# Kernel optimization log

Measured on AMD Instinct MI355X. Metric: run time of the kernel, lower is better.

The kernel has to match this reference:

```python
import jax, jax.numpy as jnp
import numpy as np

D = 256
H = 8
DH = D // H
TANH_CLIP = 10.0
NEG_INF = -1e9


def setup_inputs() -> dict:
    key = jax.random.key(0)
    ks = jax.random.split(key, 7)
    B, T, N = 32, 512, 512
    s = 1.0 / np.sqrt(D)
    return {
        "embeddings": jax.random.normal(ks[0], (B, N, D), dtype=jnp.float32),
        "current_nodes": jax.random.randint(ks[1], (B, T), 0, N, dtype=jnp.int64),
        "action_mask": jax.random.randint(ks[2], (B, T, N), 0, 2) > 0,
        "W_node": jax.random.normal(ks[3], (D, 3 * D), dtype=jnp.float32) * s,
        "W_fixed": jax.random.normal(ks[4], (D, D), dtype=jnp.float32) * s,
        "W_step": jax.random.normal(ks[5], (D, D), dtype=jnp.float32) * s,
        "W_out": jax.random.normal(ks[6], (D, D), dtype=jnp.float32) * s,
    }


def reference(embeddings, current_nodes, action_mask, W_node, W_fixed, W_step, W_out):
    """Batched equivalent of the autoregressive pointer-attention decode loop.

    embeddings: [B, N, D]; current_nodes: [B, T]; action_mask: [B, T, N] (True = feasible).
    Returns log_p: [B, T, N].
    """
    B, N, _ = embeddings.shape
    # ---- _precompute_cache ----
    proj = embeddings @ W_node                      # [B, N, 3D]
    glimpse_k, glimpse_v, logit_k = jnp.split(proj, 3, axis=-1)
    graph_context = jnp.mean(embeddings, axis=1) @ W_fixed   # [B, D]

    # ---- step context (gather current node embedding, project) ----
    step_emb = jnp.take_along_axis(embeddings, current_nodes[..., None], axis=1)  # [B, T, D]
    glimpse_q = step_emb @ W_step + graph_context[:, None, :]                      # [B, T, D]

    # ---- multi-head glimpse attention (one query per decode step) ----
    q = glimpse_q.reshape(B, -1, H, DH)
    k = glimpse_k.reshape(B, N, H, DH)
    v = glimpse_v.reshape(B, N, H, DH)
    scores = jnp.einsum("bthd,bnhd->bhtn", q, k) / np.sqrt(DH)
    scores = jnp.where(action_mask[:, None, :, :], scores, NEG_INF)
    attn = jax.nn.softmax(scores, axis=-1)
    heads = jnp.einsum("bhtn,bnhd->bthd", attn, v).reshape(B, -1, D)
    glimpse = heads @ W_out                                                        # [B, T, D]

    # ---- pointer logits: tanh clipping, mask, log-softmax ----
    logits = jnp.einsum("btd,bnd->btn", glimpse, logit_k) / np.sqrt(D)
    logits = TANH_CLIP * jnp.tanh(logits)
    logits = jnp.where(action_mask, logits, NEG_INF)
    return jax.nn.log_softmax(logits, axis=-1)
```

## Files before the change

### kernel.cpp

```cpp
#include <hip/hip_runtime.h>
#include <hip/hip_bf16.h>

constexpr int BB = 32;
constexpr int TT = 512;
constexpr int NN = 512;
constexpr int DD = 256;
constexpr int HH = 8;
constexpr int DH = 32;
#define NEG_INF (-1e9f)

typedef __attribute__((ext_vector_type(8))) short bf16x8;
typedef __attribute__((ext_vector_type(4))) float f32x4;

__device__ inline ushort f2bf(float x) {
    union { float f; unsigned u; } c; c.f = x;
    unsigned u = c.u + 0x7fffu + ((c.u >> 16) & 1u);
    return (ushort)(u >> 16);
}
__device__ inline uint pk2t(float a, float b) {
    return __builtin_amdgcn_perm(__float_as_uint(b), __float_as_uint(a),
                                 0x07060302u);
}
__device__ inline ushort tr16(float x) { return (ushort)(__float_as_uint(x) >> 16); }
__device__ inline float bf2f(ushort u) {
    union { uint u; float f; } c; c.u = (uint)u << 16; return c.f;
}
__device__ inline float fast_tanh10(float x) {
    x = fminf(fmaxf(x, -20.f), 20.f);
    float e2 = __expf(2.f * x);
    return 10.f * (1.f - 2.f / (e2 + 1.f));
}

__global__ __launch_bounds__(256) void prep_all_k(
    const float* __restrict__ emb, ushort* __restrict__ embB,
    float* __restrict__ partial, const float* __restrict__ Wn,
    const float* __restrict__ Ws, const float* __restrict__ Wo,
    ushort* __restrict__ WnT, ushort* __restrict__ WsT,
    ushort* __restrict__ WoT, const int* __restrict__ mask,
    uint* __restrict__ mbt) {
    int j = blockIdx.x;
    int tid = threadIdx.x;
    if (j < 256) {
        int b = j >> 3, part = j & 7, d = tid;
        const float* eb = emb + ((size_t)b * NN + part * 64) * DD + d;
        ushort* ob = embB + ((size_t)b * NN + part * 64) * DD + d;
        float s = 0.f;
        #pragma unroll 4
        for (int i = 0; i < 64; i++) {
            float v = eb[(size_t)i * DD];
            s += v;
            ob[(size_t)i * DD] = f2bf(v);
        }
        partial[((size_t)b * 8 + part) * DD + d] = s;
    } else if (j < 576) {
        __shared__ float t[32][33];
        int g = j - 256;
        int gx = g % 40, gy = g / 40;
        const float* W;
        ushort* WT;
        int NC, xb;
        if (gx < 24)      { W = Wn; WT = WnT; NC = 768; xb = gx; }
        else if (gx < 32) { W = Ws; WT = WsT; NC = 256; xb = gx - 24; }
        else              { W = Wo; WT = WoT; NC = 256; xb = gx - 32; }
        int tx = tid & 31, ty = tid >> 5;
        int x = xb * 32 + tx;
        int y0 = gy * 32;
        #pragma unroll
        for (int i = 0; i < 4; i++)
            t[ty + i * 8][tx] = W[(size_t)(y0 + ty + i * 8) * NC + x];
        __syncthreads();
        #pragma unroll
        for (int i = 0; i < 4; i++)
            WT[(size_t)(xb * 32 + ty + i * 8) * 256 + y0 + tx] =
                f2bf(t[tx][ty + i * 8]);
    } else {
        int idx = (j - 576) * 256 + tid;
        int row = idx >> 4, w = idx & 15;
        const int* mr = mask + (size_t)row * NN + w;
        uint u = 0;
        #pragma unroll
        for (int c = 0; c < 32; c++) u |= (uint)(mr[c * 16] != 0) << c;
        mbt[idx] = u;
    }
}

template <int TASK>
__global__ __launch_bounds__(256) void gemm3_k(
    const ushort* __restrict__ A0, const ushort* __restrict__ WT0,
    const ushort* __restrict__ WT1, ushort* __restrict__ O0,
    ushort* __restrict__ O1, ushort* __restrict__ O2,
    ushort* __restrict__ O3, const float* __restrict__ partial,
    const float* __restrict__ Wf, const int* __restrict__ cur) {
    int j = blockIdx.x;
    bool k2 = (TASK == 0) && (j >= 1536);
    int bx, by;
    if (TASK == 0 && !k2) {
        int x = j & 7, t = j >> 3;
        bx = x * 16 + t / 12; by = t % 12;
    } else {
        int jj = k2 ? j - 1536 : j;
        int x = jj & 7, t = jj >> 3;
        bx = x * 16 + (t >> 2); by = t & 3;
    }
    int row0 = bx * 128, col0 = by * 64;
    int tid = threadIdx.x;
    int w = tid >> 6, l = tid & 63;
    int lo = l & 15, hi = l >> 4;

    __shared__ ushort As[128 * 64];
    __shared__ ushort Bs[64 * 64];
    __shared__ float ctxs[64];

    const ushort* WT = k2 ? WT1 : WT0;
    const f32x4 zero = {0.f, 0.f, 0.f, 0.f};
    f32x4 acc[2][4] = {{zero, zero, zero, zero}, {zero, zero, zero, zero}};

    for (int kk = 0; kk < 4; kk++) {
        if (kk) __syncthreads();
        #pragma unroll
        for (int i = 0; i < 4; i++) {
            int u = i * 256 + tid;
            int row = u >> 3, slot = u & 7;
            int arow = row0 + row;
            const ushort* ap;
            if (k2) {
                int b = arow >> 9;
                ap = A0 + ((size_t)(b * NN + cur[arow])) * DD;
            } else {
                ap = A0 + (size_t)arow * DD;
            }
            uint4 v = *(const uint4*)(ap + kk * 64 + slot * 8);
            *(uint4*)((char*)As + row * 128 + ((slot ^ (row & 7)) << 4)) = v;
        }
        #pragma unroll
        for (int i = 0; i < 2; i++) {
            int u = i * 256 + tid;
            int row = u >> 3, slot = u & 7;
            uint4 v = *(const uint4*)(WT + (size_t)(col0 + row) * 256 + kk * 64 + slot * 8);
            *(uint4*)((char*)Bs + row * 128 + ((slot ^ (row & 7)) << 4)) = v;
        }
        __syncthreads();
        #pragma unroll
        for (int ks = 0; ks < 2; ks++) {
            int sx = ((ks * 4 + hi) ^ (lo & 7)) << 4;
            bf16x8 af0 = *(const bf16x8*)((char*)As + (w * 32 + lo) * 128 + sx);
            bf16x8 af1 = *(const bf16x8*)((char*)As + (w * 32 + 16 + lo) * 128 + sx);
            #pragma unroll
            for (int c = 0; c < 4; c++) {
                bf16x8 bf = *(const bf16x8*)((char*)Bs + (c * 16 + lo) * 128 + sx);
                acc[0][c] = __builtin_amdgcn_mfma_f32_16x16x32_bf16(af0, bf, acc[0][c], 0, 0, 0);
                acc[1][c] = __builtin_amdgcn_mfma_f32_16x16x32_bf16(af1, bf, acc[1][c], 0, 0, 0);
            }
        }
    }

    int bbq = row0 >> 9;
    if (k2) {
        __syncthreads();
        float* fs = (float*)As;
        float mk = 0.f;
        #pragma unroll
        for (int p = 0; p < 8; p++)
            mk += partial[(size_t)bbq * 2048 + p * 256 + tid];
        fs[tid] = mk * (1.0f / 512.0f);
        __syncthreads();
        int cc = tid & 63, part = tid >> 6;
        float cs = 0.f;
        #pragma unroll 16
        for (int k = part * 64; k < part * 64 + 64; k++)
            cs += fs[k] * Wf[(size_t)k * 256 + col0 + cc];
        float* fs2 = fs + 256;
        fs2[part * 64 + cc] = cs;
        __syncthreads();
        if (tid < 64)
            ctxs[tid] = fs2[tid] + fs2[64 + tid] + fs2[128 + tid] + fs2[192 + tid];
        __syncthreads();
    }

    #pragma unroll
    for (int rg = 0; rg < 2; rg++) {
        int rw0 = row0 + w * 32 + rg * 16;
        int bb = rw0 >> 9;
        #pragma unroll
        for (int c = 0; c < 4; c++) {
            int col = col0 + c * 16 + lo;
            float v[4];
            #pragma unroll
            for (int r = 0; r < 4; r++) v[r] = acc[rg][c][r];
            if constexpr (TASK == 0) {
                if (k2) {
                    float bv = ctxs[col - col0];
                    #pragma unroll
                    for (int r = 0; r < 4; r++)
                        O3[(size_t)(rw0 + 4 * hi + r) * DD + col] = f2bf(v[r] + bv);
                } else if (col < 256) {
                    int head = col >> 5, dh = col & 31;
                    #pragma unroll
                    for (int r = 0; r < 4; r++) {
                        int n = (rw0 + 4 * hi + r) & (NN - 1);
                        O0[(((size_t)(bb * HH + head) * NN + n) << 5) + dh] = f2bf(v[r]);
                    }
                } else if (col < 512) {
                    int cc2 = col - 256;
                    int bhv = bb * HH + (cc2 >> 5);
                    int dh = cc2 & 31;
                    int n0 = (rw0 + 4 * hi) & (NN - 1);
                    int m = n0 >> 2;
                    int p_ = m >> 3, s_ = (m >> 2) & 1, g_ = m & 3;
                    int n0p = (8 * p_ + 2 * g_ + s_) << 2;
                    ushort4 uv = {f2bf(v[0]), f2bf(v[1]), f2bf(v[2]), f2bf(v[3])};
                    *(ushort4*)(O1 + ((size_t)bhv * DH + dh) * NN + n0p) = uv;
                } else {
                    #pragma unroll
                    for (int r = 0; r < 4; r++)
                        O2[(size_t)(rw0 + 4 * hi + r) * 256 + (col - 512)] = f2bf(v[r]);
                }
            } else {
                #pragma unroll
                for (int r = 0; r < 4; r++)
                    O0[(size_t)(rw0 + 4 * hi + r) * DD + col] = f2bf(v[r]);
            }
        }
    }
}

__global__ __launch_bounds__(256, 4) void attn10_k(
    const ushort* __restrict__ gq, const ushort* __restrict__ gkT,
    const ushort* __restrict__ vTp, const uint* __restrict__ mbt,
    ushort* __restrict__ headsB) {
    int j = blockIdx.x;
    int bh = j & 255, quarter = j >> 8;
    int b = bh >> 3, h = bh & 7;
    int tid = threadIdx.x;
    int w = tid >> 6, l = tid & 63;
    int lo = l & 15, hi = l >> 4;

    __shared__ ushort Ks[8192];
    __shared__ ushort Vs[8192];
    __shared__ ushort OT[4][16][40];

    const f32x4 zero = {0.f, 0.f, 0.f, 0.f};
    const bf16x8 ones = {(short)0x3F80, (short)0x3F80, (short)0x3F80,
                         (short)0x3F80, (short)0x3F80, (short)0x3F80,
                         (short)0x3F80, (short)0x3F80};
    const float sc = 0.17677669529663687f;
    int q0 = quarter * 128;
    int kswz = (lo & 7) << 4;

    f32x4 o0[2] = {zero, zero};
    f32x4 o1[2] = {zero, zero};
    f32x4 osum[2] = {zero, zero};

    const char* kbase = (const char*)(gkT + (size_t)bh * (NN * DH));
    const char* vbase = (const char*)(vTp + (size_t)bh * (DH * NN));

    for (int ph = 0; ph < 2; ph++) {
        if (ph) __syncthreads();
        {
            const char* ksrc = kbase + ph * 16384;
            #pragma unroll
            for (int i = 0; i < 4; i++) {
                int u = i * 256 + tid;
                int nn = u >> 2, slot = u & 3;
                uint4 v = *(const uint4*)(ksrc + nn * 64 + slot * 16);
                *(uint4*)((char*)Ks + ((nn * 64 + slot * 16) ^ ((nn & 7) << 4))) = v;
            }
        }
        {
            const char* vsrc = vbase + ph * 512;
            #pragma unroll
            for (int i = 0; i < 4; i++) {
                int u = i * 256 + tid;
                int dh = u >> 5, slot = u & 31;
                uint4 v = *(const uint4*)(vsrc + dh * 1024 + slot * 16);
                *(uint4*)((char*)Vs + ((dh * 512 + slot * 16) ^ ((dh & 7) << 4))) = v;
            }
        }
        __syncthreads();

        #pragma unroll
        for (int qc2 = 0; qc2 < 2; qc2++) {
            int t0 = q0 + qc2 * 64 + w * 16;
            bf16x8 qf = *(const bf16x8*)(gq + ((size_t)(b * TT + t0 + lo)) * DD + h * DH + hi * 8);
            uint4 mq = *(const uint4*)(mbt + ((size_t)(b * TT + t0 + lo)) * 16 + 4 * hi);

            #pragma unroll 4
            for (int p = 0; p < 8; p++) {
                int nn = 32 * p + lo;
                bf16x8 kf0 = *(const bf16x8*)((char*)Ks + ((nn * 64 + hi * 16) ^ kswz));
                bf16x8 kf1 = *(const bf16x8*)((char*)Ks + (((nn + 16) * 64 + hi * 16) ^ kswz));
                f32x4 s0 = __builtin_amdgcn_mfma_f32_16x16x32_bf16(kf0, qf, zero, 0, 0, 0);
                f32x4 s1 = __builtin_amdgcn_mfma_f32_16x16x32_bf16(kf1, qf, zero, 0, 0, 0);
                union { bf16x8 v; uint u[4]; } pf;
                {
                    int c = ph * 16 + 2 * p;
                    float e0 = ((mq.x >> c) & 1u) ? __expf(s0[0] * sc) : 0.f;
                    float e1 = ((mq.y >> c) & 1u) ? __expf(s0[1] * sc) : 0.f;
                    float e2 = ((mq.z >> c) & 1u) ? __expf(s0[2] * sc) : 0.f;
                    float e3 = ((mq.w >> c) & 1u) ? __expf(s0[3] * sc) : 0.f;
                    pf.u[0] = pk2t(e0, e1);
                    pf.u[1] = pk2t(e2, e3);
                }
                {
                    int c = ph * 16 + 2 * p + 1;
                    float e0 = ((mq.x >> c) & 1u) ? __expf(s1[0] * sc) : 0.f;
                    float e1 = ((mq.y >> c) & 1u) ? __expf(s1[1] * sc) : 0.f;
                    float e2 = ((mq.z >> c) & 1u) ? __expf(s1[2] * sc) : 0.f;
                    float e3 = ((mq.w >> c) & 1u) ? __expf(s1[3] * sc) : 0.f;
                    pf.u[2] = pk2t(e0, e1);
                    pf.u[3] = pk2t(e2, e3);
                }
                int vo = (32 * p + 8 * hi) * 2;
                bf16x8 va0 = *(const bf16x8*)((char*)Vs + ((lo * 512 + vo) ^ kswz));
                bf16x8 va1 = *(const bf16x8*)((char*)Vs + (((lo + 16) * 512 + vo) ^ kswz));
                o0[qc2] = __builtin_amdgcn_mfma_f32_16x16x32_bf16(va0, pf.v, o0[qc2], 0, 0, 0);
                o1[qc2] = __builtin_amdgcn_mfma_f32_16x16x32_bf16(va1, pf.v, o1[qc2], 0, 0, 0);
                osum[qc2] = __builtin_amdgcn_mfma_f32_16x16x32_bf16(ones, pf.v, osum[qc2], 0, 0, 0);
            }
        }
    }

    #pragma unroll
    for (int qc2 = 0; qc2 < 2; qc2++) {
        int t0 = q0 + qc2 * 64 + w * 16;
        float inv = 1.0f / fmaxf(osum[qc2][0], 1e-30f);
        #pragma unroll
        for (int r = 0; r < 4; r++) {
            OT[w][lo][4 * hi + r] = tr16(o0[qc2][r] * inv);
            OT[w][lo][16 + 4 * hi + r] = tr16(o1[qc2][r] * inv);
        }
        bf16x8 ov = *(const bf16x8*)(&OT[w][lo][hi * 8]);
        *(bf16x8*)(headsB + ((size_t)(b * TT + t0 + lo)) * DD + h * DH + hi * 8) = ov;
    }
}

__global__ __launch_bounds__(256) void logits_mm_k(
    const ushort* __restrict__ glimpse, const ushort* __restrict__ lkb,
    const uint* __restrict__ mbt, ushort* __restrict__ logitsB,
    float* __restrict__ psum) {
    int j = blockIdx.x;
    int x = j & 7, t = j >> 3;
    int b = x * 4 + (t >> 5);
    int rem = t & 31;
    int bx = rem >> 3, by = rem & 7;
    int row0 = bx * 128, col0 = by * 64;
    int tid = threadIdx.x;
    int w = tid >> 6, l = tid & 63;
    int lo = l & 15, hi = l >> 4;

    __shared__ ushort As[128 * 64];
    __shared__ ushort Bs[64 * 64];

    const ushort* Abase = glimpse + (size_t)b * TT * DD;
    const ushort* Bbase = lkb + (size_t)b * NN * DD;

    const f32x4 zero = {0.f, 0.f, 0.f, 0.f};
    f32x4 acc[2][4] = {{zero, zero, zero, zero}, {zero, zero, zero, zero}};

    for (int kk = 0; kk < 4; kk++) {
        if (kk) __syncthreads();
        #pragma unroll
        for (int i = 0; i < 4; i++) {
            int u = i * 256 + tid;
            int row = u >> 3, slot = u & 7;
            uint4 v = *(const uint4*)(Abase + (size_t)(row0 + row) * DD + kk * 64 + slot * 8);
            *(uint4*)((char*)As + row * 128 + ((slot ^ (row & 7)) << 4)) = v;
        }
        #pragma unroll
        for (int i = 0; i < 2; i++) {
            int u = i * 256 + tid;
            int row = u >> 3, slot = u & 7;
            uint4 v = *(const uint4*)(Bbase + (size_t)(col0 + row) * DD + kk * 64 + slot * 8);
            *(uint4*)((char*)Bs + row * 128 + ((slot ^ (row & 7)) << 4)) = v;
        }
        __syncthreads();
        #pragma unroll
        for (int ks = 0; ks < 2; ks++) {
            int sx = ((ks * 4 + hi) ^ (lo & 7)) << 4;
            bf16x8 af0 = *(const bf16x8*)((char*)As + (w * 32 + lo) * 128 + sx);
            bf16x8 af1 = *(const bf16x8*)((char*)As + (w * 32 + 16 + lo) * 128 + sx);
            #pragma unroll
            for (int c = 0; c < 4; c++) {
                bf16x8 bf = *(const bf16x8*)((char*)Bs + (c * 16 + lo) * 128 + sx);
                acc[0][c] = __builtin_amdgcn_mfma_f32_16x16x32_bf16(af0, bf, acc[0][c], 0, 0, 0);
                acc[1][c] = __builtin_amdgcn_mfma_f32_16x16x32_bf16(af1, bf, acc[1][c], 0, 0, 0);
            }
        }
    }

    #pragma unroll
    for (int rg = 0; rg < 2; rg++) {
        int rw = row0 + w * 32 + rg * 16;
        uint mw[4];
        #pragma unroll
        for (int r = 0; r < 4; r++)
            mw[r] = mbt[((size_t)(b * TT + rw + 4 * hi + r)) * 16 + lo];
        float rsum[4] = {0.f, 0.f, 0.f, 0.f};
        #pragma unroll
        for (int c = 0; c < 4; c++) {
            int col = col0 + c * 16 + lo;
            int cg = by * 4 + c;
            #pragma unroll
            for (int r = 0; r < 4; r++) {
                float t2 = fast_tanh10(acc[rg][c][r] * 0.0625f);
                logitsB[((size_t)(b * TT + rw + 4 * hi + r)) * NN + col] = tr16(t2);
                rsum[r] += ((mw[r] >> cg) & 1u) ? __expf(t2 - 10.f) : 0.f;
            }
        }
        #pragma unroll
        for (int r = 0; r < 4; r++) {
            #pragma unroll
            for (int o = 1; o < 16; o <<= 1) rsum[r] += __shfl_xor(rsum[r], o);
        }
        if (lo == 0) {
            #pragma unroll
            for (int r = 0; r < 4; r++)
                psum[((size_t)(b * TT + rw + 4 * hi + r)) * 8 + by] = rsum[r];
        }
    }
}

__global__ __launch_bounds__(256) void logits_fin_k(
    const ushort* __restrict__ logitsB, const float* __restrict__ psum,
    const uint* __restrict__ mbt, float* __restrict__ out) {
    int r0 = blockIdx.x * 8;
    int tid = threadIdx.x;
    __shared__ float lsev[8];
    __shared__ uint mwv[8][16];
    if (tid < 128) {
        mwv[tid >> 4][tid & 15] = mbt[(size_t)(r0 + (tid >> 4)) * 16 + (tid & 15)];
    } else if (tid < 136) {
        int rr = tid - 128;
        const float* pp = psum + (size_t)(r0 + rr) * 8;
        float s = 0.f;
        #pragma unroll
        for (int p = 0; p < 8; p++) s += pp[p];
        lsev[rr] = 10.f + __logf(fmaxf(s, 1e-37f));
    }
    __syncthreads();
    int row = tid >> 5, n0 = (tid & 31) * 16;
    float lse = lsev[row];
    const ushort* lb = logitsB + (size_t)(r0 + row) * NN + n0;
    bf16x8 v0 = *(const bf16x8*)(lb);
    bf16x8 v1 = *(const bf16x8*)(lb + 8);
    float ov[16];
    #pragma unroll
    for (int jj = 0; jj < 16; jj++) {
        int n = n0 + jj;
        uint bit = (mwv[row][n & 15] >> (n >> 4)) & 1u;
        float lv = bf2f((ushort)(jj < 8 ? v0[jj] : v1[jj - 8]));
        ov[jj] = bit ? lv - lse : NEG_INF - lse;
    }
    float* ob = out + (size_t)(r0 + row) * NN + n0;
    #pragma unroll
    for (int q = 0; q < 4; q++)
        *(float4*)(ob + q * 4) = *(float4*)(&ov[q * 4]);
}

extern "C" void kernel_launch(void* const* d_in, const int* in_sizes, int n_in,
                              void* d_out, int out_size, void* d_ws,
                              size_t ws_size, hipStream_t stream) {
    const float* emb = (const float*)d_in[0];
    const int* cur   = (const int*)d_in[1];
    const int* mask  = (const int*)d_in[2];
    const float* Wn  = (const float*)d_in[3];
    const float* Wf  = (const float*)d_in[4];
    const float* Ws  = (const float*)d_in[5];
    const float* Wo  = (const float*)d_in[6];
    float* out = (float*)d_out;

    const size_t SLABE = (size_t)BB * NN * DD;
    ushort* embB     = (ushort*)d_ws;
    ushort* gkT      = embB + SLABE;
    ushort* vTp      = gkT + SLABE;
    ushort* lkb      = vTp + SLABE;
    ushort* gq       = lkb + SLABE;
    ushort* headsB   = gq + SLABE;
    ushort* glimpseB = headsB + SLABE;
    ushort* WnT      = glimpseB + SLABE;
    ushort* WsT      = WnT + 768 * 256;
    ushort* WoT      = WsT + 256 * 256;
    uint*   mbt      = (uint*)(WoT + 256 * 256);
    float*  partial  = (float*)(mbt + (size_t)BB * TT * 16);
    ushort* logitsB  = embB;
    float*  psum     = (float*)(embB + (size_t)BB * TT * NN);

    prep_all_k<<<1600, 256, 0, stream>>>(emb, embB, partial, Wn, Ws, Wo,
                                         WnT, WsT, WoT, mask, mbt);
    gemm3_k<0><<<2048, 256, 0, stream>>>(embB, WnT, WsT, gkT, vTp, lkb, gq,
                                         partial, Wf, cur);
    attn10_k<<<1024, 256, 0, stream>>>(gq, gkT, vTp, mbt, headsB);
    gemm3_k<1><<<512, 256, 0, stream>>>(headsB, WoT, nullptr, glimpseB,
                                        nullptr, nullptr, nullptr, nullptr,
                                        nullptr, nullptr);
    logits_mm_k<<<1024, 256, 0, stream>>>(glimpseB, lkb, mbt, logitsB, psum);
    logits_fin_k<<<BB * TT / 8, 256, 0, stream>>>(logitsB, psum, mbt, out);
}
```

Baseline: 108.4 us.

## Double-buffer GEMM tiles with direct global-to-LDS async loads

Both bf16 MFMA GEMM kernels (projection and pointer-logits) now stage A and B tiles through two LDS buffers. Loads go through global_load_lds, which writes straight into shared memory with the XOR swizzle applied on the source address instead of the destination. The next K-slice is prefetched while the current one feeds the MFMAs, which is meant to hide global load latency and drop the register round trip. In exchange LDS use doubles, which may lower occupancy, and correctness depends on waitcnt and barrier ordering of the async LDS writes.

```diff
diff --git a/kernel.cpp b/kernel.cpp
--- a/kernel.cpp
+++ b/kernel.cpp
@@ -29,6 +29,11 @@
     x = fminf(fmaxf(x, -20.f), 20.f);
     float e2 = __expf(2.f * x);
     return 10.f * (1.f - 2.f / (e2 + 1.f));
+}
+__device__ inline void gload_lds16(const void* g, void* l) {
+    __builtin_amdgcn_global_load_lds(
+        (const __attribute__((address_space(1))) unsigned int*)g,
+        (__attribute__((address_space(3))) unsigned int*)l, 16, 0, 0);
 }
 
 __global__ __launch_bounds__(256) void prep_all_k(
@@ -107,16 +112,13 @@
     int w = tid >> 6, l = tid & 63;
     int lo = l & 15, hi = l >> 4;
 
-    __shared__ ushort As[128 * 64];
-    __shared__ ushort Bs[64 * 64];
+    __shared__ ushort As[2][128 * 64];
+    __shared__ ushort Bs[2][64 * 64];
     __shared__ float ctxs[64];
 
     const ushort* WT = k2 ? WT1 : WT0;
-    const f32x4 zero = {0.f, 0.f, 0.f, 0.f};
-    f32x4 acc[2][4] = {{zero, zero, zero, zero}, {zero, zero, zero, zero}};
-
-    for (int kk = 0; kk < 4; kk++) {
-        if (kk) __syncthreads();
+
+    auto stage = [&](int buf, int kk) {
         #pragma unroll
         for (int i = 0; i < 4; i++) {
             int u = i * 256 + tid;
@@ -129,35 +131,48 @@
             } else {
                 ap = A0 + (size_t)arow * DD;
             }
-            uint4 v = *(const uint4*)(ap + kk * 64 + slot * 8);
-            *(uint4*)((char*)As + row * 128 + ((slot ^ (row & 7)) << 4)) = v;
+            const void* gsrc = ap + kk * 64 + ((slot ^ (row & 7)) << 3);
+            void* ldst = (char*)&As[buf][0] + i * 4096 + w * 1024;
+            gload_lds16(gsrc, ldst);
         }
         #pragma unroll
         for (int i = 0; i < 2; i++) {
             int u = i * 256 + tid;
             int row = u >> 3, slot = u & 7;
-            uint4 v = *(const uint4*)(WT + (size_t)(col0 + row) * 256 + kk * 64 + slot * 8);
-            *(uint4*)((char*)Bs + row * 128 + ((slot ^ (row & 7)) << 4)) = v;
-        }
-        __syncthreads();
+            const void* gsrc =
+                WT + (size_t)(col0 + row) * 256 + kk * 64 + ((slot ^ (row & 7)) << 3);
+            void* ldst = (char*)&Bs[buf][0] + i * 4096 + w * 1024;
+            gload_lds16(gsrc, ldst);
+        }
+    };
+
+    const f32x4 zero = {0.f, 0.f, 0.f, 0.f};
+    f32x4 acc[2][4] = {{zero, zero, zero, zero}, {zero, zero, zero, zero}};
+
+    stage(0, 0);
+    __syncthreads();
+    #pragma unroll
+    for (int kk = 0; kk < 4; kk++) {
+        if (kk < 3) stage((kk + 1) & 1, kk + 1);
+        int cb = kk & 1;
         #pragma unroll
         for (int ks = 0; ks < 2; ks++) {
             int sx = ((ks * 4 + hi) ^ (lo & 7)) << 4;
-            bf16x8 af0 = *(const bf16x8*)((char*)As + (w * 32 + lo) * 128 + sx);
-            bf16x8 af1 = *(const bf16x8*)((char*)As + (w * 32 + 16 + lo) * 128 + sx);
+            bf16x8 af0 = *(const bf16x8*)((char*)&As[cb][0] + (w * 32 + lo) * 128 + sx);
+            bf16x8 af1 = *(const bf16x8*)((char*)&As[cb][0] + (w * 32 + 16 + lo) * 128 + sx);
             #pragma unroll
             for (int c = 0; c < 4; c++) {
-                bf16x8 bf = *(const bf16x8*)((char*)Bs + (c * 16 + lo) * 128 + sx);
+                bf16x8 bf = *(const bf16x8*)((char*)&Bs[cb][0] + (c * 16 + lo) * 128 + sx);
                 acc[0][c] = __builtin_amdgcn_mfma_f32_16x16x32_bf16(af0, bf, acc[0][c], 0, 0, 0);
                 acc[1][c] = __builtin_amdgcn_mfma_f32_16x16x32_bf16(af1, bf, acc[1][c], 0, 0, 0);
             }
         }
+        __syncthreads();
     }
 
     int bbq = row0 >> 9;
     if (k2) {
-        __syncthreads();
-        float* fs = (float*)As;
+        float* fs = (float*)&As[0][0];
         float mk = 0.f;
         #pragma unroll
         for (int p = 0; p < 8; p++)
@@ -348,44 +363,55 @@
     int w = tid >> 6, l = tid & 63;
     int lo = l & 15, hi = l >> 4;
 
-    __shared__ ushort As[128 * 64];
-    __shared__ ushort Bs[64 * 64];
+    __shared__ ushort As[2][128 * 64];
+    __shared__ ushort Bs[2][64 * 64];
 
     const ushort* Abase = glimpse + (size_t)b * TT * DD;
     const ushort* Bbase = lkb + (size_t)b * NN * DD;
 
-    const f32x4 zero = {0.f, 0.f, 0.f, 0.f};
-    f32x4 acc[2][4] = {{zero, zero, zero, zero}, {zero, zero, zero, zero}};
-
-    for (int kk = 0; kk < 4; kk++) {
-        if (kk) __syncthreads();
+    auto stage = [&](int buf, int kk) {
         #pragma unroll
         for (int i = 0; i < 4; i++) {
             int u = i * 256 + tid;
             int row = u >> 3, slot = u & 7;
-            uint4 v = *(const uint4*)(Abase + (size_t)(row0 + row) * DD + kk * 64 + slot * 8);
-            *(uint4*)((char*)As + row * 128 + ((slot ^ (row & 7)) << 4)) = v;
+            const void* gsrc =
+                Abase + (size_t)(row0 + row) * DD + kk * 64 + ((slot ^ (row & 7)) << 3);
+            void* ldst = (char*)&As[buf][0] + i * 4096 + w * 1024;
+            gload_lds16(gsrc, ldst);
         }
         #pragma unroll
         for (int i = 0; i < 2; i++) {
             int u = i * 256 + tid;
             int row = u >> 3, slot = u & 7;
-            uint4 v = *(const uint4*)(Bbase + (size_t)(col0 + row) * DD + kk * 64 + slot * 8);
-            *(uint4*)((char*)Bs + row * 128 + ((slot ^ (row & 7)) << 4)) = v;
-        }
-        __syncthreads();
+            const void* gsrc =
+                Bbase + (size_t)(col0 + row) * DD + kk * 64 + ((slot ^ (row & 7)) << 3);
+            void* ldst = (char*)&Bs[buf][0] + i * 4096 + w * 1024;
+            gload_lds16(gsrc, ldst);
+        }
+    };
+
+    const f32x4 zero = {0.f, 0.f, 0.f, 0.f};
+    f32x4 acc[2][4] = {{zero, zero, zero, zero}, {zero, zero, zero, zero}};
+
+    stage(0, 0);
+    __syncthreads();
+    #pragma unroll
+    for (int kk = 0; kk < 4; kk++) {
+        if (kk < 3) stage((kk + 1) & 1, kk + 1);
+        int cb = kk & 1;
         #pragma unroll
         for (int ks = 0; ks < 2; ks++) {
             int sx = ((ks * 4 + hi) ^ (lo & 7)) << 4;
-            bf16x8 af0 = *(const bf16x8*)((char*)As + (w * 32 + lo) * 128 + sx);
-            bf16x8 af1 = *(const bf16x8*)((char*)As + (w * 32 + 16 + lo) * 128 + sx);
+            bf16x8 af0 = *(const bf16x8*)((char*)&As[cb][0] + (w * 32 + lo) * 128 + sx);
+            bf16x8 af1 = *(const bf16x8*)((char*)&As[cb][0] + (w * 32 + 16 + lo) * 128 + sx);
             #pragma unroll
             for (int c = 0; c < 4; c++) {
-                bf16x8 bf = *(const bf16x8*)((char*)Bs + (c * 16 + lo) * 128 + sx);
+                bf16x8 bf = *(const bf16x8*)((char*)&Bs[cb][0] + (c * 16 + lo) * 128 + sx);
                 acc[0][c] = __builtin_amdgcn_mfma_f32_16x16x32_bf16(af0, bf, acc[0][c], 0, 0, 0);
                 acc[1][c] = __builtin_amdgcn_mfma_f32_16x16x32_bf16(af1, bf, acc[1][c], 0, 0, 0);
             }
         }
+        __syncthreads();
     }
 
     #pragma unroll
```

Result: faster. 102.5 us (-5.5%).
